# Kernel tuning notes

Measured on AMD Instinct MI355X. Metric: run time of the kernel, lower is better.

Reference implementation:

```python
import jax, jax.numpy as jnp
import numpy as np

B, N, D, H = 8192, 9, 1024, 4096
# query_type '3p': num_layer=3, edges (h_ind, r_ind, t_ind), no negation, simple_graph=False
EDGES = [(2, 3, 4), (4, 5, 6), (6, 7, 8)]
NUM_LAYER = 3
EPS = 0.1


def setup_inputs() -> dict:
    key = jax.random.key(0)
    k1, k2, k3 = jax.random.split(key, 3)
    scale1 = 1.0 / np.sqrt(D)
    scale2 = 1.0 / np.sqrt(H)
    return {
        "node_embedding": jax.random.normal(k1, (B, N, D), dtype=jnp.float32),
        "W1": jax.random.normal(k2, (D, H), dtype=jnp.float32) * scale1,
        "b1": jnp.zeros((H,), dtype=jnp.float32),
        "W2": jax.random.normal(k3, (H, D), dtype=jnp.float32) * scale2,
        "b2": jnp.zeros((D,), dtype=jnp.float32),
    }


def reference(node_embedding, W1, b1, W2, b2):
    # message passing: for each edge, tail gets estimate_tail(h, r) = h + r,
    # head gets estimate_head(t, r) = t - r (mp_lhs=True, mp_rel=False).
    # The num_layer loop re-appends identical messages, so sum = NUM_LAYER * per-edge sum.
    msgs = {}
    for h, r, t in EDGES:
        he = node_embedding[:, h]   # [B, D]
        re_ = node_embedding[:, r]
        te = node_embedding[:, t]
        msgs.setdefault(t, []).append(he + re_)   # estimate_tail_emb
        msgs.setdefault(h, []).append(te - re_)   # estimate_head_emb

    def mlp(x):
        return jax.nn.relu(x @ W1 + b1) @ W2 + b2

    terms = sorted(msgs.keys())  # [2, 4, 6, 8] for '3p'
    outs = []
    for t in terms:
        agg = NUM_LAYER * sum(msgs[t]) + node_embedding[:, t] * EPS  # agg_func='sum'
        outs.append(mlp(agg))
    return jnp.stack(outs, axis=0)  # [num_terms, B, D]
```

## Files before the change

### kernel.cpp

```cpp
#include <hip/hip_runtime.h>
#include <hip/hip_bf16.h>

typedef __hip_bfloat16 bf16;
typedef __attribute__((ext_vector_type(8))) short short8;
typedef __attribute__((ext_vector_type(4))) short short4v;
typedef __attribute__((ext_vector_type(4))) float floatx4;

#define BQ 8192
#define ND 9
#define DD 1024
#define HH 4096
#define MM 32768

__device__ __forceinline__ short f2bf(float f) {
  unsigned u = __float_as_uint(f);
  u = (u + 0x7fff + ((u >> 16) & 1)) >> 16;
  return (short)u;
}

__device__ __forceinline__ void async16(const void* g, void* l) {
  __builtin_amdgcn_global_load_lds(
      (const __attribute__((address_space(1))) void*)g,
      (__attribute__((address_space(3))) void*)l, 16, 0, 0);
}

__global__ __launch_bounds__(256) void build_x(const float* __restrict__ emb,
                                               bf16* __restrict__ X) {
  int b = blockIdx.x;
  int d = threadIdx.x * 4;
  const float* base = emb + (size_t)b * (ND * DD) + d;

  float e[7][4];
#pragma unroll
  for (int k = 0; k < 7; ++k) *(float4*)e[k] = *(const float4*)(base + (k + 2) * DD);

  auto store = [&](int t, const float* v) {
    short4v o;
#pragma unroll
    for (int c = 0; c < 4; ++c) o[c] = f2bf(v[c]);
    *(short4v*)(X + ((size_t)t * BQ + b) * DD + d) = o;
  };

  float o0[4], o1[4], o2[4], o3[4];
#pragma unroll
  for (int c = 0; c < 4; ++c) {
    o0[c] = 0.1f * e[0][c] - 3.f * e[1][c] + 3.f * e[2][c];
    o1[c] = 3.f * e[0][c] + 3.f * e[1][c] + 0.1f * e[2][c] - 3.f * e[3][c] + 3.f * e[4][c];
    o2[c] = 3.f * e[2][c] + 3.f * e[3][c] + 0.1f * e[4][c] - 3.f * e[5][c] + 3.f * e[6][c];
    o3[c] = 3.f * e[4][c] + 3.f * e[5][c] + 0.1f * e[6][c];
  }
  store(0, o0); store(1, o1); store(2, o2); store(3, o3);
}

__global__ void transpose_f2b(const float* __restrict__ src, bf16* __restrict__ dst,
                              int rows, int cols) {
  __shared__ float t[32][33];
  int c0 = blockIdx.x * 32, r0 = blockIdx.y * 32;
  int tx = threadIdx.x, ty = threadIdx.y;
  t[ty][tx] = src[(size_t)(r0 + ty) * cols + (c0 + tx)];
  __syncthreads();
  short v = f2bf(t[tx][ty]);
  dst[(size_t)(c0 + ty) * rows + (r0 + tx)] = *(bf16*)&v;
}

template <int RELU, typename OutT, int K, int N, int LOGNX>
__global__ __launch_bounds__(512, 2) void gemm256(const bf16* __restrict__ A,
                                                  const bf16* __restrict__ Bt,
                                                  const float* __restrict__ bias,
                                                  OutT* __restrict__ C) {
  constexpr int NT = K / 64;
  __shared__ bf16 sm[65536];
  char* smc = (char*)sm;
  const bf16* smb = (const bf16*)sm;

  const int tid = threadIdx.x;
  const int l = tid & 63;
  const int wv = tid >> 6;

  const int G = gridDim.x;
  const int b = blockIdx.x;
  const int gb = (b & 7) * (G >> 3) + (b >> 3);
  const int n0 = (gb & ((1 << LOGNX) - 1)) * 256;
  const int m0 = (gb >> LOGNX) * 256;

  const int rowb = wv * 8 + (l >> 3);
  const int kx = ((l & 7) ^ ((l >> 3) & 7)) << 3;
  const bf16* pA = A + (size_t)(m0 + rowb) * K + kx;
  const bf16* pB = Bt + (size_t)(n0 + rowb) * K + kx;
  const int wlo = wv * 1024;

  const int ra = ((wv >> 1) * 32 + (l & 15)) * 64;
  const int rb = ((wv & 1) * 64 + (l & 15)) * 64;
  const int kg = l >> 4;
  const int sx = l & 7;

  floatx4 acc[4][8];
#pragma unroll
  for (int q = 0; q < 4; ++q)
#pragma unroll
    for (int f = 0; f < 8; ++f)
#pragma unroll
      for (int r = 0; r < 4; ++r) acc[q][f][r] = 0.f;

#define STG(GP, LO)                                            \
  do {                                                         \
    async16((GP), smc + (LO) + wlo);                           \
    async16((GP) + (size_t)64 * K, smc + (LO) + wlo + 8192);   \
  } while (0)

#define LOAD_A(HOFF)                                                          \
  _Pragma("unroll") for (int mf = 0; mf < 2; ++mf)                            \
  _Pragma("unroll") for (int ks = 0; ks < 2; ++ks)                            \
      a[mf][ks] = *(const short8*)(smb + bufe + (HOFF) + ra + mf * 1024 +     \
                                   ((((ks << 2) + kg) ^ sx) << 3));

#define LOAD_B(HOFF)                                                          \
  _Pragma("unroll") for (int nf = 0; nf < 4; ++nf)                            \
  _Pragma("unroll") for (int ks = 0; ks < 2; ++ks)                            \
      bfr[nf][ks] = *(const short8*)(smb + bufe + (HOFF) + rb + nf * 1024 +   \
                                     ((((ks << 2) + kg) ^ sx) << 3));

#define MFMA16(Q)                                                             \
  __builtin_amdgcn_s_setprio(1);                                              \
  _Pragma("unroll") for (int ks = 0; ks < 2; ++ks)                            \
  _Pragma("unroll") for (int mf = 0; mf < 2; ++mf)                            \
  _Pragma("unroll") for (int nf = 0; nf < 4; ++nf)                            \
      acc[Q][mf * 4 + nf] = __builtin_amdgcn_mfma_f32_16x16x32_bf16(          \
          a[mf][ks], bfr[nf][ks], acc[Q][mf * 4 + nf], 0, 0, 0);              \
  __builtin_amdgcn_s_setprio(0);

#define BAR() __builtin_amdgcn_s_barrier()
#define LGKM0() asm volatile("s_waitcnt lgkmcnt(0)" ::: "memory")
#define VM4() asm volatile("s_waitcnt vmcnt(4)" ::: "memory")
#define VM0() asm volatile("s_waitcnt vmcnt(0)" ::: "memory")

  STG(pB, 32768);
  STG(pA + (size_t)128 * K, 16384);
  STG(pA, 0);
  STG(pB + (size_t)128 * K, 49152);
  STG(pB + 64, 65536 + 32768);
  STG(pA + (size_t)128 * K + 64, 65536 + 16384);
  VM4();
  BAR();

  for (int t = 0; t < NT; ++t) {
    const int bufe = (t & 1) << 15;
    const int bufn = ((t + 1) & 1) << 16;
    const int bufc = (t & 1) << 16;
    short8 a[2][2], bfr[4][2];

    LOAD_A(0);
    LOAD_B(16384);
    if (t + 1 < NT) STG(pA + (size_t)(t + 1) * 64, bufn);
    BAR();
    LGKM0();
    MFMA16(0);
    BAR();

    LOAD_A(8192);
    if (t + 1 < NT) STG(pB + (size_t)128 * K + (size_t)(t + 1) * 64, bufn + 49152);
    BAR();
    LGKM0();
    MFMA16(1);
    BAR();

    LOAD_B(24576);
    if (t + 2 < NT) STG(pB + (size_t)(t + 2) * 64, bufc + 32768);
    BAR();
    LGKM0();
    MFMA16(2);
    BAR();

    LOAD_A(0);
    if (t + 2 < NT) STG(pA + (size_t)128 * K + (size_t)(t + 2) * 64, bufc + 16384);
    BAR();
    LGKM0();
    MFMA16(3);
    if (t + 2 < NT) { VM4(); } else { VM0(); }
    BAR();
  }

  const int col0 = n0 + (wv & 1) * 64 + (l & 15);
  const int row0 = m0 + (wv >> 1) * 32 + ((l >> 4) << 2);
#pragma unroll
  for (int q = 0; q < 4; ++q) {
    const int qa = (q == 1 || q == 2) ? 1 : 0;
    const int qb = (q >= 2) ? 1 : 0;
#pragma unroll
    for (int nf = 0; nf < 4; ++nf) {
      const int col = col0 + qb * 128 + nf * 16;
      const float bv = bias[col];
#pragma unroll
      for (int mf = 0; mf < 2; ++mf) {
#pragma unroll
        for (int r = 0; r < 4; ++r) {
          const int row = row0 + qa * 128 + mf * 16 + r;
          float v = acc[q][mf * 4 + nf][r] + bv;
          if (RELU) v = fmaxf(v, 0.f);
          if constexpr (sizeof(OutT) == 2) {
            short s = f2bf(v);
            C[(size_t)row * N + col] = *(OutT*)&s;
          } else {
            C[(size_t)row * N + col] = *(OutT*)&v;
          }
        }
      }
    }
  }
#undef STG
#undef LOAD_A
#undef LOAD_B
#undef MFMA16
#undef BAR
#undef LGKM0
#undef VM4
#undef VM0
}

extern "C" void kernel_launch(void* const* d_in, const int* in_sizes, int n_in,
                              void* d_out, int out_size, void* d_ws, size_t ws_size,
                              hipStream_t stream) {
  const float* emb = (const float*)d_in[0];
  const float* W1  = (const float*)d_in[1];
  const float* b1  = (const float*)d_in[2];
  const float* W2  = (const float*)d_in[3];
  const float* b2  = (const float*)d_in[4];
  float* out = (float*)d_out;

  char* ws = (char*)d_ws;
  bf16* X   = (bf16*)(ws);
  bf16* Y   = (bf16*)(ws + (size_t)67108864);
  bf16* W1t = (bf16*)(ws + (size_t)67108864 + (size_t)268435456);
  bf16* W2t = (bf16*)(ws + (size_t)67108864 + (size_t)268435456 + (size_t)8388608);

  build_x<<<dim3(BQ), dim3(256), 0, stream>>>(emb, X);
  transpose_f2b<<<dim3(HH / 32, DD / 32), dim3(32, 32), 0, stream>>>(W1, W1t, DD, HH);
  transpose_f2b<<<dim3(DD / 32, HH / 32), dim3(32, 32), 0, stream>>>(W2, W2t, HH, DD);
  gemm256<1, bf16, DD, HH, 4><<<dim3((MM / 256) * (HH / 256)), dim3(512), 0, stream>>>(X, W1t, b1, Y);
  gemm256<0, float, HH, DD, 2><<<dim3((MM / 256) * (DD / 256)), dim3(512), 0, stream>>>(Y, W2t, b2, out);
}
```

Measured before the change: 930.2 us.

## Simplify GEMM main loop to whole-tile double buffering with one barrier

Replaces the four-phase, finely interleaved LDS pipeline with a plain two-buffer scheme. Each K-tile now reads all A and B fragments up front, issues the async loads for the next tile into the other buffer, runs all four MFMA quadrants, and ends with a single __syncthreads. This removes eight barriers and the explicit waitcnt choreography per tile, cutting synchronisation overhead. In exchange, prefetch distance shrinks to one tile, the end-of-tile barrier likely drains all outstanding global loads, and more fragment registers stay live at once.

```diff
diff --git a/kernel.cpp b/kernel.cpp
--- a/kernel.cpp
+++ b/kernel.cpp
@@ -78,8 +78,8 @@
   const int wv = tid >> 6;
 
   const int G = gridDim.x;
-  const int b = blockIdx.x;
-  const int gb = (b & 7) * (G >> 3) + (b >> 3);
+  const int bid = blockIdx.x;
+  const int gb = (bid & 7) * (G >> 3) + (bid >> 3);
   const int n0 = (gb & ((1 << LOGNX) - 1)) * 256;
   const int m0 = (gb >> LOGNX) * 256;
 
@@ -108,76 +108,58 @@
     async16((GP) + (size_t)64 * K, smc + (LO) + wlo + 8192);   \
   } while (0)
 
-#define LOAD_A(HOFF)                                                          \
-  _Pragma("unroll") for (int mf = 0; mf < 2; ++mf)                            \
-  _Pragma("unroll") for (int ks = 0; ks < 2; ++ks)                            \
-      a[mf][ks] = *(const short8*)(smb + bufe + (HOFF) + ra + mf * 1024 +     \
-                                   ((((ks << 2) + kg) ^ sx) << 3));
-
-#define LOAD_B(HOFF)                                                          \
-  _Pragma("unroll") for (int nf = 0; nf < 4; ++nf)                            \
-  _Pragma("unroll") for (int ks = 0; ks < 2; ++ks)                            \
-      bfr[nf][ks] = *(const short8*)(smb + bufe + (HOFF) + rb + nf * 1024 +   \
+#define RD_A(dst, REG, BUFE)                                                   \
+  _Pragma("unroll") for (int mf = 0; mf < 2; ++mf)                             \
+  _Pragma("unroll") for (int ks = 0; ks < 2; ++ks)                             \
+      dst[mf][ks] = *(const short8*)(smb + (BUFE) + (REG) + ra + mf * 1024 +   \
                                      ((((ks << 2) + kg) ^ sx) << 3));
 
-#define MFMA16(Q)                                                             \
-  __builtin_amdgcn_s_setprio(1);                                              \
-  _Pragma("unroll") for (int ks = 0; ks < 2; ++ks)                            \
-  _Pragma("unroll") for (int mf = 0; mf < 2; ++mf)                            \
-  _Pragma("unroll") for (int nf = 0; nf < 4; ++nf)                            \
-      acc[Q][mf * 4 + nf] = __builtin_amdgcn_mfma_f32_16x16x32_bf16(          \
-          a[mf][ks], bfr[nf][ks], acc[Q][mf * 4 + nf], 0, 0, 0);              \
+#define RD_B(dst, REG, BUFE)                                                   \
+  _Pragma("unroll") for (int nf = 0; nf < 4; ++nf)                             \
+  _Pragma("unroll") for (int ks = 0; ks < 2; ++ks)                             \
+      dst[nf][ks] = *(const short8*)(smb + (BUFE) + (REG) + rb + nf * 1024 +   \
+                                     ((((ks << 2) + kg) ^ sx) << 3));
+
+#define MF(AF, BF, Q)                                                          \
+  __builtin_amdgcn_s_setprio(1);                                               \
+  _Pragma("unroll") for (int ks = 0; ks < 2; ++ks)                             \
+  _Pragma("unroll") for (int mf = 0; mf < 2; ++mf)                             \
+  _Pragma("unroll") for (int nf = 0; nf < 4; ++nf)                             \
+      acc[Q][mf * 4 + nf] = __builtin_amdgcn_mfma_f32_16x16x32_bf16(           \
+          AF[mf][ks], BF[nf][ks], acc[Q][mf * 4 + nf], 0, 0, 0);               \
   __builtin_amdgcn_s_setprio(0);
 
-#define BAR() __builtin_amdgcn_s_barrier()
-#define LGKM0() asm volatile("s_waitcnt lgkmcnt(0)" ::: "memory")
-#define VM4() asm volatile("s_waitcnt vmcnt(4)" ::: "memory")
-#define VM0() asm volatile("s_waitcnt vmcnt(0)" ::: "memory")
-
+#define TILE(tt, EC, BN)                                                       \
+  do {                                                                         \
+    short8 a0[2][2], a1[2][2], b0[4][2], b1[4][2];                             \
+    RD_A(a0, 0, EC);                                                           \
+    RD_B(b0, 16384, EC);                                                       \
+    RD_A(a1, 8192, EC);                                                        \
+    RD_B(b1, 24576, EC);                                                       \
+    if ((tt) + 1 < NT) {                                                       \
+      const size_t ko = (size_t)((tt) + 1) * 64;                               \
+      STG(pA + ko, BN);                                                        \
+      STG(pA + (size_t)128 * K + ko, (BN) + 16384);                            \
+      STG(pB + ko, (BN) + 32768);                                              \
+      STG(pB + (size_t)128 * K + ko, (BN) + 49152);                            \
+    }                                                                          \
+    MF(a0, b0, 0);                                                             \
+    MF(a1, b0, 1);                                                             \
+    MF(a1, b1, 2);                                                             \
+    MF(a0, b1, 3);                                                             \
+    __syncthreads();                                                           \
+  } while (0)
+
+  STG(pA, 0);
+  STG(pA + (size_t)128 * K, 16384);
   STG(pB, 32768);
-  STG(pA + (size_t)128 * K, 16384);
-  STG(pA, 0);
   STG(pB + (size_t)128 * K, 49152);
-  STG(pB + 64, 65536 + 32768);
-  STG(pA + (size_t)128 * K + 64, 65536 + 16384);
-  VM4();
-  BAR();
-
-  for (int t = 0; t < NT; ++t) {
-    const int bufe = (t & 1) << 15;
-    const int bufn = ((t + 1) & 1) << 16;
-    const int bufc = (t & 1) << 16;
-    short8 a[2][2], bfr[4][2];
-
-    LOAD_A(0);
-    LOAD_B(16384);
-    if (t + 1 < NT) STG(pA + (size_t)(t + 1) * 64, bufn);
-    BAR();
-    LGKM0();
-    MFMA16(0);
-    BAR();
-
-    LOAD_A(8192);
-    if (t + 1 < NT) STG(pB + (size_t)128 * K + (size_t)(t + 1) * 64, bufn + 49152);
-    BAR();
-    LGKM0();
-    MFMA16(1);
-    BAR();
-
-    LOAD_B(24576);
-    if (t + 2 < NT) STG(pB + (size_t)(t + 2) * 64, bufc + 32768);
-    BAR();
-    LGKM0();
-    MFMA16(2);
-    BAR();
-
-    LOAD_A(0);
-    if (t + 2 < NT) STG(pA + (size_t)128 * K + (size_t)(t + 2) * 64, bufc + 16384);
-    BAR();
-    LGKM0();
-    MFMA16(3);
-    if (t + 2 < NT) { VM4(); } else { VM0(); }
-    BAR();
+  __syncthreads();
+
+#pragma unroll 1
+  for (int t = 0; t < NT; t += 2) {
+    TILE(t, 0, 65536);
+    TILE(t + 1, 32768, 0);
   }
 
   const int col0 = n0 + (wv & 1) * 64 + (l & 15);
@@ -208,13 +190,10 @@
     }
   }
 #undef STG
-#undef LOAD_A
-#undef LOAD_B
-#undef MFMA16
-#undef BAR
-#undef LGKM0
-#undef VM4
-#undef VM0
+#undef RD_A
+#undef RD_B
+#undef MF
+#undef TILE
 }
 
 extern "C" void kernel_launch(void* const* d_in, const int* in_sizes, int n_in,
```

New measurement: 1.141 ms. 22.7% more time.
